# Kernel optimization log

Hardware: AMD Instinct MI355X
Metric: run time of the kernel (lower is better)

The kernel has to match this reference:

```python
import jax, jax.numpy as jnp
import numpy as np
import math

B, P, N = 4, 8, 512
D_MODEL, H, D_K = 128, 4, 32
T_ALL = 4
WHICH_IDX = np.array([0, 1, 3])  # which_transition_matrices = [T,T,F,T]
T = 3
EPS = 1e-5


def setup_inputs() -> dict:
    key = jax.random.key(0)
    ks = jax.random.split(key, 12)
    inputs = jax.random.normal(ks[0], (B, P, N, D_MODEL), jnp.float32)
    c_inputs = jax.random.normal(ks[1], (B, P, N, D_MODEL), jnp.float32)
    vals = jax.random.uniform(ks[2], (T_ALL, N, N), jnp.float32)
    keep = (jax.random.uniform(ks[3], (T_ALL, N, N)) < 0.05).astype(jnp.float32)
    eye = jnp.eye(N, dtype=jnp.float32)
    transition_matrices = vals * keep * (1.0 - eye) + eye
    s = 1.0 / math.sqrt(D_MODEL)
    Wq = jax.random.normal(ks[4], (T, D_MODEL, D_MODEL), jnp.float32) * s
    Wk = jax.random.normal(ks[5], (T, D_MODEL, D_MODEL), jnp.float32) * s
    Wv = jax.random.normal(ks[6], (T, D_MODEL, D_MODEL), jnp.float32) * s
    Wo = jax.random.normal(ks[7], (D_MODEL, T * D_MODEL), jnp.float32) * (1.0 / math.sqrt(T * D_MODEL))
    ln_gamma = jnp.ones((D_MODEL,), jnp.float32)
    ln_beta = jnp.zeros((D_MODEL,), jnp.float32)
    return dict(inputs=inputs, c_inputs=c_inputs, transition_matrices=transition_matrices,
                Wq=Wq, Wk=Wk, Wv=Wv, Wo=Wo, ln_gamma=ln_gamma, ln_beta=ln_beta)


def reference(inputs, c_inputs, transition_matrices, Wq, Wk, Wv, Wo, ln_gamma, ln_beta):
    tm = transition_matrices[jnp.asarray(WHICH_IDX)]  # [T, N, N]
    # per-transition-matrix projections (torch Linear: x @ W.T), then split heads
    def proj(W):
        y = jnp.einsum('bpnd,tod->tbpno', inputs, W)
        return y.reshape(T, B, P, N, H, D_K)
    Q, K, V = proj(Wq), proj(Wk), proj(Wv)
    scores = jnp.einsum('tbpnhk,tbpmhk->tbphnm', Q, K) / math.sqrt(D_K)
    mask = jnp.where(tm != 0, 0.0, -jnp.inf)[:, None, None, None]  # [T,1,1,1,N,N]
    alpha = jax.nn.softmax(scores + mask, axis=-1)
    # post-softmax reweighting by transition matrix, then V matmul
    out = jnp.einsum('tbphnm,tbpmhk->tbpnhk', alpha * tm[:, None, None, None], V)
    out = out.reshape(T, B, P, N, D_MODEL)
    out = jnp.moveaxis(out, 0, -2).reshape(B, P, N, T * D_MODEL)  # concat over matrices
    out = jnp.einsum('bpnf,df->bpnd', out, Wo)  # final Linear (bias=False); dropout p=0
    res = out + inputs
    mu = res.mean(-1, keepdims=True)
    var = ((res - mu) ** 2).mean(-1, keepdims=True)
    return (res - mu) / jnp.sqrt(var + EPS) * ln_gamma + ln_beta
```

## Files before the change

### kernel.cpp

```cpp
#include <hip/hip_runtime.h>


typedef __attribute__((ext_vector_type(8))) short  short8;
typedef __attribute__((ext_vector_type(4))) float  floatx4;

#define WS_BIG   50331648ull
#define QSCALE   0.25503486f

__device__ __forceinline__ unsigned short f2b(float f) {
    union { float f; unsigned int i; } v; v.f = f;
    unsigned int x = v.i;
    return (unsigned short)((x + 0x7fffu + ((x >> 16) & 1u)) >> 16);
}
__device__ __forceinline__ unsigned int fbits(float f) {
    union { float f; unsigned int i; } v; v.f = f; return v.i;
}
__device__ __forceinline__ short8 cvt8(const float* p) {
    floatx4 a = *(const floatx4*)p;
    floatx4 b = *(const floatx4*)(p + 4);
    short8 r;
    r[0] = (short)f2b(a[0]); r[1] = (short)f2b(a[1]);
    r[2] = (short)f2b(a[2]); r[3] = (short)f2b(a[3]);
    r[4] = (short)f2b(b[0]); r[5] = (short)f2b(b[1]);
    r[6] = (short)f2b(b[2]); r[7] = (short)f2b(b[3]);
    return r;
}

__global__ __launch_bounds__(256) void k_qkv_cvt(
    const float* __restrict__ X,
    const float* __restrict__ Wq, const float* __restrict__ Wk,
    const float* __restrict__ Wv,
    unsigned short* __restrict__ q_ws, unsigned short* __restrict__ k_ws,
    unsigned short* __restrict__ v_ws,
    int wstride, int ostride)
{
    int bp = blockIdx.x, mt = blockIdx.y, tz = blockIdx.z;
    __shared__ unsigned short Xs[128 * 128];
    int tid = threadIdx.x;
    int lane = tid & 63, wv = tid >> 6;
    int l15 = lane & 15, quad = lane >> 4;

    const float* Xbase = X + ((size_t)bp * 512 + mt * 128) * 128;
    for (int i = 0; i < 8; ++i) {
        int e = (i * 256 + tid) * 8;
        *(short8*)&Xs[e] = cvt8(&Xbase[e]);
    }
    __syncthreads();

    size_t woff = (size_t)tz * wstride;
    size_t ooff = (size_t)tz * ostride;
    const float* Wsel[3] = { Wq + woff, Wk + woff, Wv + woff };
    unsigned short* Osel[3] = { q_ws + ooff, k_ws + ooff, v_ws + ooff };

    for (int qkv = 0; qkv < 3; ++qkv) {
        const float* Wt = Wsel[qkv];
        unsigned short* Ob = Osel[qkv] + ((size_t)bp * 512 + mt * 128) * 128;
        float sc = (qkv == 0) ? QSCALE : 1.0f;
        for (int ct = 0; ct < 8; ++ct) {
            short8 bfr[4];
            for (int kk = 0; kk < 4; ++kk)
                bfr[kk] = cvt8(&Wt[(size_t)(ct * 16 + l15) * 128 + kk * 32 + quad * 8]);
            floatx4 acc0 = {0.f, 0.f, 0.f, 0.f};
            floatx4 acc1 = {0.f, 0.f, 0.f, 0.f};
            int rt0 = wv * 2, rt1 = wv * 2 + 1;
            for (int kk = 0; kk < 4; ++kk) {
                short8 a0 = *(const short8*)&Xs[(rt0 * 16 + l15) * 128 + kk * 32 + quad * 8];
                short8 a1 = *(const short8*)&Xs[(rt1 * 16 + l15) * 128 + kk * 32 + quad * 8];
                acc0 = __builtin_amdgcn_mfma_f32_16x16x32_bf16(a0, bfr[kk], acc0, 0, 0, 0);
                acc1 = __builtin_amdgcn_mfma_f32_16x16x32_bf16(a1, bfr[kk], acc1, 0, 0, 0);
            }
            int col = ct * 16 + l15;
            for (int i = 0; i < 4; ++i) {
                Ob[(size_t)(rt0 * 16 + quad * 4 + i) * 128 + col] = f2b(acc0[i] * sc);
                Ob[(size_t)(rt1 * 16 + quad * 4 + i) * 128 + col] = f2b(acc1[i] * sc);
            }
        }
    }
}

__global__ __launch_bounds__(512) void k_attn4(
    const unsigned short* __restrict__ q_ws,
    const unsigned short* __restrict__ k_ws,
    const unsigned short* __restrict__ v_ws,
    const float* __restrict__ tm,
    unsigned short* __restrict__ att_ws,
    int qkv_stride, int toff0)
{
    int nc2 = blockIdx.x;
    int bp = blockIdx.y;
    int z  = blockIdx.z;
    int t = z >> 2, h = z & 3;
    size_t qoff = (size_t)t * (size_t)qkv_stride;
    const float* tmt = tm + (size_t)(t + (t >> 1)) * 262144;
    int toff = toff0 + t * 128;

    __shared__ unsigned short Vt[32][516];
    __shared__ unsigned short Ps[8][16][72];

    int tid = threadIdx.x, lane = tid & 63, wv = tid >> 6;
    int l15 = lane & 15, quad = lane >> 4;

    {
        const unsigned short* vp = v_ws + qoff + ((size_t)bp * 512 + tid) * 128 + h * 32;
        short8 a = *(const short8*)vp;
        short8 b = *(const short8*)(vp + 8);
        short8 c = *(const short8*)(vp + 16);
        short8 d = *(const short8*)(vp + 24);
        #pragma unroll
        for (int j = 0; j < 8; ++j) {
            Vt[j][tid]      = (unsigned short)a[j];
            Vt[8 + j][tid]  = (unsigned short)b[j];
            Vt[16 + j][tid] = (unsigned short)c[j];
            Vt[24 + j][tid] = (unsigned short)d[j];
        }
    }
    int n0 = nc2 * 256 + wv * 16;
    short8 qf[2];
    qf[0] = *(const short8*)&q_ws[qoff +
        ((size_t)bp * 512 + n0 + l15) * 128 + h * 32 + quad * 8];
    qf[1] = *(const short8*)&q_ws[qoff +
        ((size_t)bp * 512 + n0 + 128 + l15) * 128 + h * 32 + quad * 8];
    __syncthreads();

    const unsigned short* Kb = k_ws + qoff + (size_t)bp * 512 * 128 + h * 32;
    const float* tpc = tmt + (size_t)(n0 + quad * 4) * 512 + l15;

    floatx4 O0[2] = {{0.f,0.f,0.f,0.f},{0.f,0.f,0.f,0.f}};
    floatx4 O1[2] = {{0.f,0.f,0.f,0.f},{0.f,0.f,0.f,0.f}};
    float za[2][4] = {{0.f,0.f,0.f,0.f},{0.f,0.f,0.f,0.f}};
    const floatx4 zero4 = {0.f, 0.f, 0.f, 0.f};

    float tmA[16], tmB[16];
    #pragma unroll
    for (int ti = 0; ti < 4; ++ti)
        #pragma unroll
        for (int i = 0; i < 4; ++i)
            tmA[ti * 4 + i] = tpc[i * 512 + ti * 16];

    for (int c = 0; c < 8; ++c) {
        int mb = c * 64;
        short8 kf0 = *(const short8*)&Kb[(size_t)(mb +  0 + l15) * 128 + quad * 8];
        short8 kf1 = *(const short8*)&Kb[(size_t)(mb + 16 + l15) * 128 + quad * 8];
        short8 kf2 = *(const short8*)&Kb[(size_t)(mb + 32 + l15) * 128 + quad * 8];
        short8 kf3 = *(const short8*)&Kb[(size_t)(mb + 48 + l15) * 128 + quad * 8];

        #pragma unroll
        for (int ti = 0; ti < 4; ++ti)
            #pragma unroll
            for (int i = 0; i < 4; ++i)
                tmB[ti * 4 + i] = tpc[(128 + i) * 512 + ti * 16];
        {
            floatx4 S[4];
            S[0] = __builtin_amdgcn_mfma_f32_16x16x32_bf16(qf[0], kf0, zero4, 0, 0, 0);
            S[1] = __builtin_amdgcn_mfma_f32_16x16x32_bf16(qf[0], kf1, zero4, 0, 0, 0);
            S[2] = __builtin_amdgcn_mfma_f32_16x16x32_bf16(qf[0], kf2, zero4, 0, 0, 0);
            S[3] = __builtin_amdgcn_mfma_f32_16x16x32_bf16(qf[0], kf3, zero4, 0, 0, 0);
            #pragma unroll
            for (int ti = 0; ti < 4; ++ti) {
                #pragma unroll
                for (int i = 0; i < 4; ++i) {
                    float tmv = tmA[ti * 4 + i];
                    float e = __builtin_amdgcn_exp2f(S[ti][i]);
                    za[0][i] += (tmv != 0.0f) ? e : 0.0f;
                    float w = e * tmv;
                    Ps[wv][quad * 4 + i][ti * 16 + l15] =
                        (unsigned short)((fbits(w) + 0x8000u) >> 16);
                }
            }
            #pragma unroll
            for (int kc = 0; kc < 2; ++kc) {
                short8 pa  = *(const short8*)&Ps[wv][l15][kc * 32 + quad * 8];
                short8 vb0 = *(const short8*)&Vt[l15][mb + kc * 32 + quad * 8];
                short8 vb1 = *(const short8*)&Vt[16 + l15][mb + kc * 32 + quad * 8];
                O0[0] = __builtin_amdgcn_mfma_f32_16x16x32_bf16(pa, vb0, O0[0], 0, 0, 0);
                O1[0] = __builtin_amdgcn_mfma_f32_16x16x32_bf16(pa, vb1, O1[0], 0, 0, 0);
            }
        }

        #pragma unroll
        for (int ti = 0; ti < 4; ++ti)
            #pragma unroll
            for (int i = 0; i < 4; ++i)
                tmA[ti * 4 + i] = tpc[i * 512 + 64 + ti * 16];
        {
            floatx4 S[4];
            S[0] = __builtin_amdgcn_mfma_f32_16x16x32_bf16(qf[1], kf0, zero4, 0, 0, 0);
            S[1] = __builtin_amdgcn_mfma_f32_16x16x32_bf16(qf[1], kf1, zero4, 0, 0, 0);
            S[2] = __builtin_amdgcn_mfma_f32_16x16x32_bf16(qf[1], kf2, zero4, 0, 0, 0);
            S[3] = __builtin_amdgcn_mfma_f32_16x16x32_bf16(qf[1], kf3, zero4, 0, 0, 0);
            #pragma unroll
            for (int ti = 0; ti < 4; ++ti) {
                #pragma unroll
                for (int i = 0; i < 4; ++i) {
                    float tmv = tmB[ti * 4 + i];
                    float e = __builtin_amdgcn_exp2f(S[ti][i]);
                    za[1][i] += (tmv != 0.0f) ? e : 0.0f;
                    float w = e * tmv;
                    Ps[wv][quad * 4 + i][ti * 16 + l15] =
                        (unsigned short)((fbits(w) + 0x8000u) >> 16);
                }
            }
            #pragma unroll
            for (int kc = 0; kc < 2; ++kc) {
                short8 pa  = *(const short8*)&Ps[wv][l15][kc * 32 + quad * 8];
                short8 vb0 = *(const short8*)&Vt[l15][mb + kc * 32 + quad * 8];
                short8 vb1 = *(const short8*)&Vt[16 + l15][mb + kc * 32 + quad * 8];
                O0[1] = __builtin_amdgcn_mfma_f32_16x16x32_bf16(pa, vb0, O0[1], 0, 0, 0);
                O1[1] = __builtin_amdgcn_mfma_f32_16x16x32_bf16(pa, vb1, O1[1], 0, 0, 0);
            }
        }
        tpc += 64;
    }

    #pragma unroll
    for (int s = 0; s < 2; ++s) {
        #pragma unroll
        for (int d = 1; d < 16; d <<= 1) {
            #pragma unroll
            for (int i = 0; i < 4; ++i) za[s][i] += __shfl_xor(za[s][i], d, 64);
        }
        #pragma unroll
        for (int i = 0; i < 4; ++i) {
            float rz = 1.0f / za[s][i];
            size_t row = (size_t)bp * 512 + n0 + s * 128 + quad * 4 + i;
            att_ws[row * 384 + toff + h * 32 + l15]      = f2b(O0[s][i] * rz);
            att_ws[row * 384 + toff + h * 32 + 16 + l15] = f2b(O1[s][i] * rz);
        }
    }
}

__global__ __launch_bounds__(256) void k_oproj_cvt(
    const unsigned short* __restrict__ att_ws,
    const float* __restrict__ Wo,
    const float* __restrict__ X,
    const float* __restrict__ gamma,
    const float* __restrict__ beta,
    float* __restrict__ out)
{
    int bp = blockIdx.x;
    int mt = blockIdx.y;
    __shared__ unsigned short As[64 * 128];
    __shared__ unsigned short Ws[128 * 128];
    int tid = threadIdx.x, lane = tid & 63, wv = tid >> 6;
    int l15 = lane & 15, quad = lane >> 4;

    floatx4 acc[8];
    for (int ct = 0; ct < 8; ++ct) acc[ct] = (floatx4){0.f, 0.f, 0.f, 0.f};
    size_t rowbase = (size_t)bp * 512 + mt * 64;

    for (int kc = 0; kc < 3; ++kc) {
        __syncthreads();
        for (int i = 0; i < 4; ++i) {
            int flat = i * 256 + tid;
            int row = flat >> 4, colg = (flat & 15) * 8;
            *(short8*)&As[row * 128 + colg] =
                *(const short8*)&att_ws[(rowbase + row) * 384 + kc * 128 + colg];
        }
        for (int i = 0; i < 8; ++i) {
            int flat = i * 256 + tid;
            int row = flat >> 4, colg = (flat & 15) * 8;
            *(short8*)&Ws[row * 128 + colg] = cvt8(&Wo[(size_t)row * 384 + kc * 128 + colg]);
        }
        __syncthreads();
        for (int ct = 0; ct < 8; ++ct) {
            for (int kk = 0; kk < 4; ++kk) {
                short8 a = *(const short8*)&As[(wv * 16 + l15) * 128 + kk * 32 + quad * 8];
                short8 b = *(const short8*)&Ws[(ct * 16 + l15) * 128 + kk * 32 + quad * 8];
                acc[ct] = __builtin_amdgcn_mfma_f32_16x16x32_bf16(a, b, acc[ct], 0, 0, 0);
            }
        }
    }

    for (int i = 0; i < 4; ++i) {
        int lrow = wv * 16 + quad * 4 + i;
        size_t grow = rowbase + lrow;
        float vals[8];
        float s = 0.f, sq = 0.f;
        for (int ct = 0; ct < 8; ++ct) {
            int col = ct * 16 + l15;
            float v = acc[ct][i] + X[grow * 128 + col];
            vals[ct] = v;
            s += v; sq += v * v;
        }
        for (int d = 1; d < 16; d <<= 1) {
            s  += __shfl_xor(s, d, 64);
            sq += __shfl_xor(sq, d, 64);
        }
        float mu = s * (1.0f / 128.0f);
        float var = sq * (1.0f / 128.0f) - mu * mu;
        float rs = rsqrtf(var + 1e-5f);
        for (int ct = 0; ct < 8; ++ct) {
            int col = ct * 16 + l15;
            out[grow * 128 + col] = (vals[ct] - mu) * rs * gamma[col] + beta[col];
        }
    }
}

extern "C" void kernel_launch(void* const* d_in, const int* in_sizes, int n_in,
                              void* d_out, int out_size, void* d_ws, size_t ws_size,
                              hipStream_t stream) {
    const float* X     = (const float*)d_in[0];
    const float* TM    = (const float*)d_in[2];
    const float* Wq    = (const float*)d_in[3];
    const float* Wk    = (const float*)d_in[4];
    const float* Wv    = (const float*)d_in[5];
    const float* Wo    = (const float*)d_in[6];
    const float* gamma = (const float*)d_in[7];
    const float* beta  = (const float*)d_in[8];
    float* out = (float*)d_out;

    char* ws = (char*)d_ws;
    const size_t QKV1 = 2097152;
    const size_t QKV1B = QKV1 * 2;

    if (ws_size >= WS_BIG) {
        unsigned short* q3  = (unsigned short*)(ws);
        unsigned short* k3  = (unsigned short*)(ws + 3 * QKV1B);
        unsigned short* v3  = (unsigned short*)(ws + 6 * QKV1B);
        unsigned short* att = (unsigned short*)(ws + 9 * QKV1B);
        k_qkv_cvt<<<dim3(32, 4, 3), 256, 0, stream>>>(
            X, Wq, Wk, Wv, q3, k3, v3, 16384, (int)QKV1);
        k_attn4<<<dim3(2, 32, 12), 512, 0, stream>>>(q3, k3, v3, TM, att, (int)QKV1, 0);
        k_oproj_cvt<<<dim3(32, 8), 256, 0, stream>>>(att, Wo, X, gamma, beta, out);
    } else {
        unsigned short* q_ws   = (unsigned short*)(ws);
        unsigned short* k_ws   = (unsigned short*)(ws + QKV1B);
        unsigned short* v_ws   = (unsigned short*)(ws + 2 * QKV1B);
        unsigned short* att_ws = (unsigned short*)(ws + 3 * QKV1B);
        const int tsel[3] = {0, 1, 3};
        for (int t = 0; t < 3; ++t) {
            k_qkv_cvt<<<dim3(32, 4, 1), 256, 0, stream>>>(
                X, Wq + (size_t)t * 16384, Wk + (size_t)t * 16384, Wv + (size_t)t * 16384,
                q_ws, k_ws, v_ws, 0, 0);
            k_attn4<<<dim3(2, 32, 4), 512, 0, stream>>>(
                q_ws, k_ws, v_ws, TM + (size_t)tsel[t] * 262144, att_ws, 0, t * 128);
        }
        k_oproj_cvt<<<dim3(32, 8), 256, 0, stream>>>(att_ws, Wo, X, gamma, beta, out);
    }
}
```

Before: 197.5 us.

## Split QKV projection across nine blocks per tile with LDS-staged coalesced stores

```diff
diff --git a/kernel.cpp b/kernel.cpp
--- a/kernel.cpp
+++ b/kernel.cpp
@@ -24,6 +24,288 @@
     r[4] = (short)f2b(b[0]); r[5] = (short)f2b(b[1]);
     r[6] = (short)f2b(b[2]); r[7] = (short)f2b(b[3]);
     return r;
+}
+
+__global__ __launch_bounds__(256) void k_qkv_fused(
+    const float* __restrict__ X,
+    const float* __restrict__ Wq,
+    const float* __restrict__ Wk,
+    const float* __restrict__ Wv,
+    unsigned short* __restrict__ q_ws,
+    unsigned short* __restrict__ k_ws,
+    unsigned short* __restrict__ v_ws)
+{
+    int bp = blockIdx.x, mt = blockIdx.y, z = blockIdx.z;
+    int qkv = z / 3, t = z % 3;
+    __shared__ unsigned short Xs[128 * 128];
+    __shared__ unsigned short Cs[4][32 * 128];
+    int tid = threadIdx.x;
+    int lane = tid & 63, wv = tid >> 6;
+    int l15 = lane & 15, quad = lane >> 4;
+
+    const float* Xbase = X + ((size_t)bp * 512 + mt * 128) * 128;
+    for (int i = 0; i < 8; ++i) {
+        int e = (i * 256 + tid) * 8;
+        *(short8*)&Xs[e] = cvt8(&Xbase[e]);
+    }
+    __syncthreads();
+
+    const float* Wsel[3] = { Wq, Wk, Wv };
+    unsigned short* Osel[3] = { q_ws, k_ws, v_ws };
+    int rt0 = wv * 2, rt1 = wv * 2 + 1;
+
+    const float* Wt = Wsel[qkv] + (size_t)t * 16384;
+    unsigned short* Ob = Osel[qkv] + (size_t)t * 2097152
+                       + ((size_t)bp * 512 + mt * 128 + wv * 32) * 128;
+    float sc = (qkv == 0) ? QSCALE : 1.0f;
+
+    for (int ct = 0; ct < 8; ++ct) {
+        short8 bfr[4];
+        for (int kk = 0; kk < 4; ++kk)
+            bfr[kk] = cvt8(&Wt[(size_t)(ct * 16 + l15) * 128 + kk * 32 + quad * 8]);
+        floatx4 acc0 = {0.f, 0.f, 0.f, 0.f};
+        floatx4 acc1 = {0.f, 0.f, 0.f, 0.f};
+        for (int kk = 0; kk < 4; ++kk) {
+            short8 a0 = *(const short8*)&Xs[(rt0 * 16 + l15) * 128 + kk * 32 + quad * 8];
+            short8 a1 = *(const short8*)&Xs[(rt1 * 16 + l15) * 128 + kk * 32 + quad * 8];
+            acc0 = __builtin_amdgcn_mfma_f32_16x16x32_bf16(a0, bfr[kk], acc0, 0, 0, 0);
+            acc1 = __builtin_amdgcn_mfma_f32_16x16x32_bf16(a1, bfr[kk], acc1, 0, 0, 0);
+        }
+        #pragma unroll
+        for (int i = 0; i < 4; ++i) {
+            int row = quad * 4 + i;
+            int swz = (row & 7) << 4;
+            int col = (ct * 16 + l15) ^ swz;
+            Cs[wv][row * 128 + col]        = f2b(acc0[i] * sc);
+            Cs[wv][(16 + row) * 128 + col] = f2b(acc1[i] * sc);
+        }
+    }
+    #pragma unroll
+    for (int j = 0; j < 8; ++j) {
+        int flat = j * 64 + lane;
+        int r = flat >> 4;
+        int cg = (flat & 15) * 8;
+        int cgs = cg ^ ((r & 7) << 4);
+        *(short8*)&Ob[(size_t)r * 128 + cg] = *(const short8*)&Cs[wv][r * 128 + cgs];
+    }
+}
+
+__global__ __launch_bounds__(512) void k_attn4(
+    const unsigned short* __restrict__ q_ws,
+    const unsigned short* __restrict__ k_ws,
+    const unsigned short* __restrict__ v_ws,
+    const float* __restrict__ tm,
+    unsigned short* __restrict__ att_ws,
+    int qkv_stride, int toff0)
+{
+    int nc2 = blockIdx.x;
+    int bp = blockIdx.y;
+    int z  = blockIdx.z;
+    int t = z >> 2, h = z & 3;
+    size_t qoff = (size_t)t * (size_t)qkv_stride;
+    const float* tmt = tm + (size_t)(t + (t >> 1)) * 262144;
+    int toff = toff0 + t * 128;
+
+    __shared__ unsigned short Vt[32][516];
+    __shared__ unsigned short Ps[8][16][72];
+
+    int tid = threadIdx.x, lane = tid & 63, wv = tid >> 6;
+    int l15 = lane & 15, quad = lane >> 4;
+
+    {
+        const unsigned short* vp = v_ws + qoff + ((size_t)bp * 512 + tid) * 128 + h * 32;
+        short8 a = *(const short8*)vp;
+        short8 b = *(const short8*)(vp + 8);
+        short8 c = *(const short8*)(vp + 16);
+        short8 d = *(const short8*)(vp + 24);
+        #pragma unroll
+        for (int j = 0; j < 8; ++j) {
+            Vt[j][tid]      = (unsigned short)a[j];
+            Vt[8 + j][tid]  = (unsigned short)b[j];
+            Vt[16 + j][tid] = (unsigned short)c[j];
+            Vt[24 + j][tid] = (unsigned short)d[j];
+        }
+    }
+    int n0 = nc2 * 256 + wv * 16;
+    short8 qf[2];
+    qf[0] = *(const short8*)&q_ws[qoff +
+        ((size_t)bp * 512 + n0 + l15) * 128 + h * 32 + quad * 8];
+    qf[1] = *(const short8*)&q_ws[qoff +
+        ((size_t)bp * 512 + n0 + 128 + l15) * 128 + h * 32 + quad * 8];
+    __syncthreads();
+
+    const unsigned short* Kb = k_ws + qoff + (size_t)bp * 512 * 128 + h * 32;
+    const float* tpc = tmt + (size_t)(n0 + quad * 4) * 512 + l15;
+
+    floatx4 O0[2] = {{0.f,0.f,0.f,0.f},{0.f,0.f,0.f,0.f}};
+    floatx4 O1[2] = {{0.f,0.f,0.f,0.f},{0.f,0.f,0.f,0.f}};
+    float za[2][4] = {{0.f,0.f,0.f,0.f},{0.f,0.f,0.f,0.f}};
+    const floatx4 zero4 = {0.f, 0.f, 0.f, 0.f};
+
+    float tmA[16], tmB[16];
+    #pragma unroll
+    for (int ti = 0; ti < 4; ++ti)
+        #pragma unroll
+        for (int i = 0; i < 4; ++i)
+            tmA[ti * 4 + i] = tpc[i * 512 + ti * 16];
+
+    for (int c = 0; c < 8; ++c) {
+        int mb = c * 64;
+        short8 kf0 = *(const short8*)&Kb[(size_t)(mb +  0 + l15) * 128 + quad * 8];
+        short8 kf1 = *(const short8*)&Kb[(size_t)(mb + 16 + l15) * 128 + quad * 8];
+        short8 kf2 = *(const short8*)&Kb[(size_t)(mb + 32 + l15) * 128 + quad * 8];
+        short8 kf3 = *(const short8*)&Kb[(size_t)(mb + 48 + l15) * 128 + quad * 8];
+
+        #pragma unroll
+        for (int ti = 0; ti < 4; ++ti)
+            #pragma unroll
+            for (int i = 0; i < 4; ++i)
+                tmB[ti * 4 + i] = tpc[(128 + i) * 512 + ti * 16];
+        {
+            floatx4 S[4];
+            S[0] = __builtin_amdgcn_mfma_f32_16x16x32_bf16(qf[0], kf0, zero4, 0, 0, 0);
+            S[1] = __builtin_amdgcn_mfma_f32_16x16x32_bf16(qf[0], kf1, zero4, 0, 0, 0);
+            S[2] = __builtin_amdgcn_mfma_f32_16x16x32_bf16(qf[0], kf2, zero4, 0, 0, 0);
+            S[3] = __builtin_amdgcn_mfma_f32_16x16x32_bf16(qf[0], kf3, zero4, 0, 0, 0);
+            #pragma unroll
+            for (int ti = 0; ti < 4; ++ti) {
+                #pragma unroll
+                for (int i = 0; i < 4; ++i) {
+                    float tmv = tmA[ti * 4 + i];
+                    float e = __builtin_amdgcn_exp2f(S[ti][i]);
+                    za[0][i] += (tmv != 0.0f) ? e : 0.0f;
+                    float w = e * tmv;
+                    Ps[wv][quad * 4 + i][ti * 16 + l15] =
+                        (unsigned short)((fbits(w) + 0x8000u) >> 16);
+                }
+            }
+            #pragma unroll
+            for (int kc = 0; kc < 2; ++kc) {
+                short8 pa  = *(const short8*)&Ps[wv][l15][kc * 32 + quad * 8];
+                short8 vb0 = *(const short8*)&Vt[l15][mb + kc * 32 + quad * 8];
+                short8 vb1 = *(const short8*)&Vt[16 + l15][mb + kc * 32 + quad * 8];
+                O0[0] = __builtin_amdgcn_mfma_f32_16x16x32_bf16(pa, vb0, O0[0], 0, 0, 0);
+                O1[0] = __builtin_amdgcn_mfma_f32_16x16x32_bf16(pa, vb1, O1[0], 0, 0, 0);
+            }
+        }
+
+        #pragma unroll
+        for (int ti = 0; ti < 4; ++ti)
+            #pragma unroll
+            for (int i = 0; i < 4; ++i)
+                tmA[ti * 4 + i] = tpc[i * 512 + 64 + ti * 16];
+        {
+            floatx4 S[4];
+            S[0] = __builtin_amdgcn_mfma_f32_16x16x32_bf16(qf[1], kf0, zero4, 0, 0, 0);
+            S[1] = __builtin_amdgcn_mfma_f32_16x16x32_bf16(qf[1], kf1, zero4, 0, 0, 0);
+            S[2] = __builtin_amdgcn_mfma_f32_16x16x32_bf16(qf[1], kf2, zero4, 0, 0, 0);
+            S[3] = __builtin_amdgcn_mfma_f32_16x16x32_bf16(qf[1], kf3, zero4, 0, 0, 0);
+            #pragma unroll
+            for (int ti = 0; ti < 4; ++ti) {
+                #pragma unroll
+                for (int i = 0; i < 4; ++i) {
+                    float tmv = tmB[ti * 4 + i];
+                    float e = __builtin_amdgcn_exp2f(S[ti][i]);
+                    za[1][i] += (tmv != 0.0f) ? e : 0.0f;
+                    float w = e * tmv;
+                    Ps[wv][quad * 4 + i][ti * 16 + l15] =
+                        (unsigned short)((fbits(w) + 0x8000u) >> 16);
+                }
+            }
+            #pragma unroll
+            for (int kc = 0; kc < 2; ++kc) {
+                short8 pa  = *(const short8*)&Ps[wv][l15][kc * 32 + quad * 8];
+                short8 vb0 = *(const short8*)&Vt[l15][mb + kc * 32 + quad * 8];
+                short8 vb1 = *(const short8*)&Vt[16 + l15][mb + kc * 32 + quad * 8];
+                O0[1] = __builtin_amdgcn_mfma_f32_16x16x32_bf16(pa, vb0, O0[1], 0, 0, 0);
+                O1[1] = __builtin_amdgcn_mfma_f32_16x16x32_bf16(pa, vb1, O1[1], 0, 0, 0);
+            }
+        }
+        tpc += 64;
+    }
+
+    #pragma unroll
+    for (int s = 0; s < 2; ++s) {
+        #pragma unroll
+        for (int d = 1; d < 16; d <<= 1) {
+            #pragma unroll
+            for (int i = 0; i < 4; ++i) za[s][i] += __shfl_xor(za[s][i], d, 64);
+        }
+        #pragma unroll
+        for (int i = 0; i < 4; ++i) {
+            float rz = 1.0f / za[s][i];
+            size_t row = (size_t)bp * 512 + n0 + s * 128 + quad * 4 + i;
+            att_ws[row * 384 + toff + h * 32 + l15]      = f2b(O0[s][i] * rz);
+            att_ws[row * 384 + toff + h * 32 + 16 + l15] = f2b(O1[s][i] * rz);
+        }
+    }
+}
+
+__global__ __launch_bounds__(256) void k_oproj_cvt(
+    const unsigned short* __restrict__ att_ws,
+    const float* __restrict__ Wo,
+    const float* __restrict__ X,
+    const float* __restrict__ gamma,
+    const float* __restrict__ beta,
+    float* __restrict__ out)
+{
+    int bp = blockIdx.x;
+    int mt = blockIdx.y;
+    __shared__ unsigned short As[64 * 128];
+    __shared__ unsigned short Ws[128 * 128];
+    int tid = threadIdx.x, lane = tid & 63, wv = tid >> 6;
+    int l15 = lane & 15, quad = lane >> 4;
+
+    floatx4 acc[8];
+    for (int ct = 0; ct < 8; ++ct) acc[ct] = (floatx4){0.f, 0.f, 0.f, 0.f};
+    size_t rowbase = (size_t)bp * 512 + mt * 64;
+
+    for (int kc = 0; kc < 3; ++kc) {
+        __syncthreads();
+        for (int i = 0; i < 4; ++i) {
+            int flat = i * 256 + tid;
+            int row = flat >> 4, colg = (flat & 15) * 8;
+            *(short8*)&As[row * 128 + colg] =
+                *(const short8*)&att_ws[(rowbase + row) * 384 + kc * 128 + colg];
+        }
+        for (int i = 0; i < 8; ++i) {
+            int flat = i * 256 + tid;
+            int row = flat >> 4, colg = (flat & 15) * 8;
+            *(short8*)&Ws[row * 128 + colg] = cvt8(&Wo[(size_t)row * 384 + kc * 128 + colg]);
+        }
+        __syncthreads();
+        for (int ct = 0; ct < 8; ++ct) {
+            for (int kk = 0; kk < 4; ++kk) {
+                short8 a = *(const short8*)&As[(wv * 16 + l15) * 128 + kk * 32 + quad * 8];
+                short8 b = *(const short8*)&Ws[(ct * 16 + l15) * 128 + kk * 32 + quad * 8];
+                acc[ct] = __builtin_amdgcn_mfma_f32_16x16x32_bf16(a, b, acc[ct], 0, 0, 0);
+            }
+        }
+    }
+
+    for (int i = 0; i < 4; ++i) {
+        int lrow = wv * 16 + quad * 4 + i;
+        size_t grow = rowbase + lrow;
+        float vals[8];
+        float s = 0.f, sq = 0.f;
+        for (int ct = 0; ct < 8; ++ct) {
+            int col = ct * 16 + l15;
+            float v = acc[ct][i] + X[grow * 128 + col];
+            vals[ct] = v;
+            s += v; sq += v * v;
+        }
+        for (int d = 1; d < 16; d <<= 1) {
+            s  += __shfl_xor(s, d, 64);
+            sq += __shfl_xor(sq, d, 64);
+        }
+        float mu = s * (1.0f / 128.0f);
+        float var = sq * (1.0f / 128.0f) - mu * mu;
+        float rs = rsqrtf(var + 1e-5f);
+        for (int ct = 0; ct < 8; ++ct) {
+            int col = ct * 16 + l15;
+            out[grow * 128 + col] = (vals[ct] - mu) * rs * gamma[col] + beta[col];
+        }
+    }
 }
 
 __global__ __launch_bounds__(256) void k_qkv_cvt(
@@ -78,224 +360,6 @@
     }
 }
 
-__global__ __launch_bounds__(512) void k_attn4(
-    const unsigned short* __restrict__ q_ws,
-    const unsigned short* __restrict__ k_ws,
-    const unsigned short* __restrict__ v_ws,
-    const float* __restrict__ tm,
-    unsigned short* __restrict__ att_ws,
-    int qkv_stride, int toff0)
-{
-    int nc2 = blockIdx.x;
-    int bp = blockIdx.y;
-    int z  = blockIdx.z;
-    int t = z >> 2, h = z & 3;
-    size_t qoff = (size_t)t * (size_t)qkv_stride;
-    const float* tmt = tm + (size_t)(t + (t >> 1)) * 262144;
-    int toff = toff0 + t * 128;
-
-    __shared__ unsigned short Vt[32][516];
-    __shared__ unsigned short Ps[8][16][72];
-
-    int tid = threadIdx.x, lane = tid & 63, wv = tid >> 6;
-    int l15 = lane & 15, quad = lane >> 4;
-
-    {
-        const unsigned short* vp = v_ws + qoff + ((size_t)bp * 512 + tid) * 128 + h * 32;
-        short8 a = *(const short8*)vp;
-        short8 b = *(const short8*)(vp + 8);
-        short8 c = *(const short8*)(vp + 16);
-        short8 d = *(const short8*)(vp + 24);
-        #pragma unroll
-        for (int j = 0; j < 8; ++j) {
-            Vt[j][tid]      = (unsigned short)a[j];
-            Vt[8 + j][tid]  = (unsigned short)b[j];
-            Vt[16 + j][tid] = (unsigned short)c[j];
-            Vt[24 + j][tid] = (unsigned short)d[j];
-        }
-    }
-    int n0 = nc2 * 256 + wv * 16;
-    short8 qf[2];
-    qf[0] = *(const short8*)&q_ws[qoff +
-        ((size_t)bp * 512 + n0 + l15) * 128 + h * 32 + quad * 8];
-    qf[1] = *(const short8*)&q_ws[qoff +
-        ((size_t)bp * 512 + n0 + 128 + l15) * 128 + h * 32 + quad * 8];
-    __syncthreads();
-
-    const unsigned short* Kb = k_ws + qoff + (size_t)bp * 512 * 128 + h * 32;
-    const float* tpc = tmt + (size_t)(n0 + quad * 4) * 512 + l15;
-
-    floatx4 O0[2] = {{0.f,0.f,0.f,0.f},{0.f,0.f,0.f,0.f}};
-    floatx4 O1[2] = {{0.f,0.f,0.f,0.f},{0.f,0.f,0.f,0.f}};
-    float za[2][4] = {{0.f,0.f,0.f,0.f},{0.f,0.f,0.f,0.f}};
-    const floatx4 zero4 = {0.f, 0.f, 0.f, 0.f};
-
-    float tmA[16], tmB[16];
-    #pragma unroll
-    for (int ti = 0; ti < 4; ++ti)
-        #pragma unroll
-        for (int i = 0; i < 4; ++i)
-            tmA[ti * 4 + i] = tpc[i * 512 + ti * 16];
-
-    for (int c = 0; c < 8; ++c) {
-        int mb = c * 64;
-        short8 kf0 = *(const short8*)&Kb[(size_t)(mb +  0 + l15) * 128 + quad * 8];
-        short8 kf1 = *(const short8*)&Kb[(size_t)(mb + 16 + l15) * 128 + quad * 8];
-        short8 kf2 = *(const short8*)&Kb[(size_t)(mb + 32 + l15) * 128 + quad * 8];
-        short8 kf3 = *(const short8*)&Kb[(size_t)(mb + 48 + l15) * 128 + quad * 8];
-
-        #pragma unroll
-        for (int ti = 0; ti < 4; ++ti)
-            #pragma unroll
-            for (int i = 0; i < 4; ++i)
-                tmB[ti * 4 + i] = tpc[(128 + i) * 512 + ti * 16];
-        {
-            floatx4 S[4];
-            S[0] = __builtin_amdgcn_mfma_f32_16x16x32_bf16(qf[0], kf0, zero4, 0, 0, 0);
-            S[1] = __builtin_amdgcn_mfma_f32_16x16x32_bf16(qf[0], kf1, zero4, 0, 0, 0);
-            S[2] = __builtin_amdgcn_mfma_f32_16x16x32_bf16(qf[0], kf2, zero4, 0, 0, 0);
-            S[3] = __builtin_amdgcn_mfma_f32_16x16x32_bf16(qf[0], kf3, zero4, 0, 0, 0);
-            #pragma unroll
-            for (int ti = 0; ti < 4; ++ti) {
-                #pragma unroll
-                for (int i = 0; i < 4; ++i) {
-                    float tmv = tmA[ti * 4 + i];
-                    float e = __builtin_amdgcn_exp2f(S[ti][i]);
-                    za[0][i] += (tmv != 0.0f) ? e : 0.0f;
-                    float w = e * tmv;
-                    Ps[wv][quad * 4 + i][ti * 16 + l15] =
-                        (unsigned short)((fbits(w) + 0x8000u) >> 16);
-                }
-            }
-            #pragma unroll
-            for (int kc = 0; kc < 2; ++kc) {
-                short8 pa  = *(const short8*)&Ps[wv][l15][kc * 32 + quad * 8];
-                short8 vb0 = *(const short8*)&Vt[l15][mb + kc * 32 + quad * 8];
-                short8 vb1 = *(const short8*)&Vt[16 + l15][mb + kc * 32 + quad * 8];
-                O0[0] = __builtin_amdgcn_mfma_f32_16x16x32_bf16(pa, vb0, O0[0], 0, 0, 0);
-                O1[0] = __builtin_amdgcn_mfma_f32_16x16x32_bf16(pa, vb1, O1[0], 0, 0, 0);
-            }
-        }
-
-        #pragma unroll
-        for (int ti = 0; ti < 4; ++ti)
-            #pragma unroll
-            for (int i = 0; i < 4; ++i)
-                tmA[ti * 4 + i] = tpc[i * 512 + 64 + ti * 16];
-        {
-            floatx4 S[4];
-            S[0] = __builtin_amdgcn_mfma_f32_16x16x32_bf16(qf[1], kf0, zero4, 0, 0, 0);
-            S[1] = __builtin_amdgcn_mfma_f32_16x16x32_bf16(qf[1], kf1, zero4, 0, 0, 0);
-            S[2] = __builtin_amdgcn_mfma_f32_16x16x32_bf16(qf[1], kf2, zero4, 0, 0, 0);
-            S[3] = __builtin_amdgcn_mfma_f32_16x16x32_bf16(qf[1], kf3, zero4, 0, 0, 0);
-            #pragma unroll
-            for (int ti = 0; ti < 4; ++ti) {
-                #pragma unroll
-                for (int i = 0; i < 4; ++i) {
-                    float tmv = tmB[ti * 4 + i];
-                    float e = __builtin_amdgcn_exp2f(S[ti][i]);
-                    za[1][i] += (tmv != 0.0f) ? e : 0.0f;
-                    float w = e * tmv;
-                    Ps[wv][quad * 4 + i][ti * 16 + l15] =
-                        (unsigned short)((fbits(w) + 0x8000u) >> 16);
-                }
-            }
-            #pragma unroll
-            for (int kc = 0; kc < 2; ++kc) {
-                short8 pa  = *(const short8*)&Ps[wv][l15][kc * 32 + quad * 8];
-                short8 vb0 = *(const short8*)&Vt[l15][mb + kc * 32 + quad * 8];
-                short8 vb1 = *(const short8*)&Vt[16 + l15][mb + kc * 32 + quad * 8];
-                O0[1] = __builtin_amdgcn_mfma_f32_16x16x32_bf16(pa, vb0, O0[1], 0, 0, 0);
-                O1[1] = __builtin_amdgcn_mfma_f32_16x16x32_bf16(pa, vb1, O1[1], 0, 0, 0);
-            }
-        }
-        tpc += 64;
-    }
-
-    #pragma unroll
-    for (int s = 0; s < 2; ++s) {
-        #pragma unroll
-        for (int d = 1; d < 16; d <<= 1) {
-            #pragma unroll
-            for (int i = 0; i < 4; ++i) za[s][i] += __shfl_xor(za[s][i], d, 64);
-        }
-        #pragma unroll
-        for (int i = 0; i < 4; ++i) {
-            float rz = 1.0f / za[s][i];
-            size_t row = (size_t)bp * 512 + n0 + s * 128 + quad * 4 + i;
-            att_ws[row * 384 + toff + h * 32 + l15]      = f2b(O0[s][i] * rz);
-            att_ws[row * 384 + toff + h * 32 + 16 + l15] = f2b(O1[s][i] * rz);
-        }
-    }
-}
-
-__global__ __launch_bounds__(256) void k_oproj_cvt(
-    const unsigned short* __restrict__ att_ws,
-    const float* __restrict__ Wo,
-    const float* __restrict__ X,
-    const float* __restrict__ gamma,
-    const float* __restrict__ beta,
-    float* __restrict__ out)
-{
-    int bp = blockIdx.x;
-    int mt = blockIdx.y;
-    __shared__ unsigned short As[64 * 128];
-    __shared__ unsigned short Ws[128 * 128];
-    int tid = threadIdx.x, lane = tid & 63, wv = tid >> 6;
-    int l15 = lane & 15, quad = lane >> 4;
-
-    floatx4 acc[8];
-    for (int ct = 0; ct < 8; ++ct) acc[ct] = (floatx4){0.f, 0.f, 0.f, 0.f};
-    size_t rowbase = (size_t)bp * 512 + mt * 64;
-
-    for (int kc = 0; kc < 3; ++kc) {
-        __syncthreads();
-        for (int i = 0; i < 4; ++i) {
-            int flat = i * 256 + tid;
-            int row = flat >> 4, colg = (flat & 15) * 8;
-            *(short8*)&As[row * 128 + colg] =
-                *(const short8*)&att_ws[(rowbase + row) * 384 + kc * 128 + colg];
-        }
-        for (int i = 0; i < 8; ++i) {
-            int flat = i * 256 + tid;
-            int row = flat >> 4, colg = (flat & 15) * 8;
-            *(short8*)&Ws[row * 128 + colg] = cvt8(&Wo[(size_t)row * 384 + kc * 128 + colg]);
-        }
-        __syncthreads();
-        for (int ct = 0; ct < 8; ++ct) {
-            for (int kk = 0; kk < 4; ++kk) {
-                short8 a = *(const short8*)&As[(wv * 16 + l15) * 128 + kk * 32 + quad * 8];
-                short8 b = *(const short8*)&Ws[(ct * 16 + l15) * 128 + kk * 32 + quad * 8];
-                acc[ct] = __builtin_amdgcn_mfma_f32_16x16x32_bf16(a, b, acc[ct], 0, 0, 0);
-            }
-        }
-    }
-
-    for (int i = 0; i < 4; ++i) {
-        int lrow = wv * 16 + quad * 4 + i;
-        size_t grow = rowbase + lrow;
-        float vals[8];
-        float s = 0.f, sq = 0.f;
-        for (int ct = 0; ct < 8; ++ct) {
-            int col = ct * 16 + l15;
-            float v = acc[ct][i] + X[grow * 128 + col];
-            vals[ct] = v;
-            s += v; sq += v * v;
-        }
-        for (int d = 1; d < 16; d <<= 1) {
-            s  += __shfl_xor(s, d, 64);
-            sq += __shfl_xor(sq, d, 64);
-        }
-        float mu = s * (1.0f / 128.0f);
-        float var = sq * (1.0f / 128.0f) - mu * mu;
-        float rs = rsqrtf(var + 1e-5f);
-        for (int ct = 0; ct < 8; ++ct) {
-            int col = ct * 16 + l15;
-            out[grow * 128 + col] = (vals[ct] - mu) * rs * gamma[col] + beta[col];
-        }
-    }
-}
-
 extern "C" void kernel_launch(void* const* d_in, const int* in_sizes, int n_in,
                               void* d_out, int out_size, void* d_ws, size_t ws_size,
                               hipStream_t stream) {
@@ -318,8 +382,7 @@
         unsigned short* k3  = (unsigned short*)(ws + 3 * QKV1B);
         unsigned short* v3  = (unsigned short*)(ws + 6 * QKV1B);
         unsigned short* att = (unsigned short*)(ws + 9 * QKV1B);
-        k_qkv_cvt<<<dim3(32, 4, 3), 256, 0, stream>>>(
-            X, Wq, Wk, Wv, q3, k3, v3, 16384, (int)QKV1);
+        k_qkv_fused<<<dim3(32, 4, 9), 256, 0, stream>>>(X, Wq, Wk, Wv, q3, k3, v3);
         k_attn4<<<dim3(2, 32, 12), 512, 0, stream>>>(q3, k3, v3, TM, att, (int)QKV1, 0);
         k_oproj_cvt<<<dim3(32, 8), 256, 0, stream>>>(att, Wo, X, gamma, beta, out);
     } else {
```

Measured after the change: 190.6 us. 1.04x faster.
